# Optimization experiments

Hardware: AMD Instinct MI355X
Metric: run time of the kernel (lower is better)

The kernel has to match this reference:

```python
import jax, jax.numpy as jnp
import numpy as np
from jax import lax

DIM = 192; K = 3; SHARE_PLANES = 8
B = 2; D = 16; H = 32; W = 32
GROUPS_W = DIM * K * K // SHARE_PLANES // (K ** 3)   # 8 dynamic-weight groups
SHARE = DIM // GROUPS_W                              # 24 channels share each group
GN_GROUPS = DIM // SHARE_PLANES                      # 24 GroupNorm groups over 216 ch
ATTN = max(DIM * 2 // 4, 32)                         # 96 SE hidden channels
EPS = 1e-5


def setup_inputs() -> dict:
    key = jax.random.key(0)
    ks = jax.random.split(key, 24)
    rn = lambda k, sh, s=0.05: jax.random.normal(k, sh, jnp.float32) * s
    sc = lambda k, sh: 1.0 + jax.random.uniform(k, sh, jnp.float32) * 0.1
    return {
        'x':      jax.random.normal(ks[0], (B, DIM, D, H, W), jnp.float32),
        'w_key':  rn(ks[1], (DIM, DIM // 4, K, K, K)),
        'bn1_s':  sc(ks[2], (DIM,)),  'bn1_b': rn(ks[3], (DIM,)),
        'w_e1':   rn(ks[4], (DIM // 2, 2 * DIM)),
        'bn2_s':  sc(ks[5], (DIM // 2,)), 'bn2_b': rn(ks[6], (DIM // 2,)),
        'w_e2':   rn(ks[7], (K * K * DIM // SHARE_PLANES, DIM // 2)),
        'b_e2':   rn(ks[8], (K * K * DIM // SHARE_PLANES,)),
        'gn_s':   sc(ks[9], (K * K * DIM // SHARE_PLANES,)),
        'gn_b':   rn(ks[10], (K * K * DIM // SHARE_PLANES,)),
        'w_c1':   rn(ks[11], (DIM, DIM)),
        'bn3_s':  sc(ks[12], (DIM,)), 'bn3_b': rn(ks[13], (DIM,)),
        'bn4_s':  sc(ks[14], (DIM,)), 'bn4_b': rn(ks[15], (DIM,)),
        'w_se1':  rn(ks[16], (ATTN, DIM)), 'b_se1': rn(ks[17], (ATTN,)),
        'bnse_s': sc(ks[18], (ATTN,)), 'bnse_b': rn(ks[19], (ATTN,)),
        'w_se2':  rn(ks[20], (2 * DIM, ATTN)), 'b_se2': rn(ks[21], (2 * DIM,)),
    }


def _bn5(t, s, b):  # eval-mode BatchNorm3d folded to per-channel affine
    return t * s[None, :, None, None, None] + b[None, :, None, None, None]


def _conv1x1(w, t):  # pointwise Conv3d as contraction over channels
    return jnp.einsum('oi,bidhw->bodhw', w, t)


def reference(x, w_key, bn1_s, bn1_b, w_e1, bn2_s, bn2_b, w_e2, b_e2, gn_s, gn_b,
              w_c1, bn3_s, bn3_b, bn4_s, bn4_b, w_se1, b_se1, bnse_s, bnse_b,
              w_se2, b_se2):
    # key embedding: grouped 3x3x3 conv + BN + ReLU
    k = lax.conv_general_dilated(x, w_key, (1, 1, 1), 'SAME',
                                 dimension_numbers=('NCDHW', 'OIDHW', 'NCDHW'),
                                 feature_group_count=4)
    k = jax.nn.relu(_bn5(k, bn1_s, bn1_b))

    qk = jnp.concatenate([x, k], axis=1)                    # [B, 2C, D, H, W]
    e = jax.nn.relu(_bn5(_conv1x1(w_e1, qk), bn2_s, bn2_b)) # [B, C/2, D, H, W]
    w = _conv1x1(w_e2, e) + b_e2[None, :, None, None, None] # [B, 216, D, H, W]

    # GroupNorm over 24 groups of 9 channels
    b_, cw, d_, h_, w_ = w.shape
    wg = w.reshape(b_, GN_GROUPS, cw // GN_GROUPS, d_, h_, w_)
    mu = wg.mean(axis=(2, 3, 4, 5), keepdims=True)
    var = wg.var(axis=(2, 3, 4, 5), keepdims=True)
    w = ((wg - mu) * lax.rsqrt(var + EPS)).reshape(b_, cw, d_, h_, w_)
    w = w * gn_s[None, :, None, None, None] + gn_b[None, :, None, None, None]

    # dynamic per-pixel weights: [B, G=8, K^3=27, D, H, W]
    wdyn = w.reshape(b_, GROUPS_W, K ** 3, d_, h_, w_)

    v = _bn5(_conv1x1(w_c1, x), bn3_s, bn3_b)               # values [B, C, D, H, W]

    # LocalConvolution (involution): accumulate over 27 shifts, never
    # materializing the full [B, C, 27, D, H, W] unfold.
    pad = (K - 1) // 2
    vpad = jnp.pad(v, ((0, 0), (0, 0), (pad, pad), (pad, pad), (pad, pad)))
    out = jnp.zeros_like(v)
    idx = 0
    for dz in range(K):
        for dy in range(K):
            for dx in range(K):
                patch = vpad[:, :, dz:dz + d_, dy:dy + h_, dx:dx + w_]
                wk = jnp.repeat(wdyn[:, :, idx], SHARE, axis=1)  # [B, C, D, H, W]
                out = out + wk * patch
                idx += 1

    x2 = _bn5(out, bn4_s, bn4_b)
    x2 = x2 * jax.nn.sigmoid(x2)                             # swish

    stacked = jnp.stack([x2, k], axis=2)                     # [B, C, radix=2, D, H, W]
    gap = stacked.sum(axis=2).mean(axis=(2, 3, 4))           # [B, C]
    h1 = jax.nn.relu((jnp.einsum('oi,bi->bo', w_se1, gap) + b_se1) * bnse_s + bnse_b)
    attn = jnp.einsum('oi,bi->bo', w_se2, h1) + b_se2        # [B, 2C]
    attn = jax.nn.softmax(attn.reshape(b_, DIM, 2), axis=2)
    return (stacked * attn[:, :, :, None, None, None]).sum(axis=2)
```

## Files before the change

### kernel.cpp

```cpp
#include <hip/hip_runtime.h>
#include <hip/hip_bf16.h>
#include <cstdint>

#define SP 16384

typedef __attribute__((ext_vector_type(8))) short bf16x8;
typedef __attribute__((ext_vector_type(4))) short bf16x4;
typedef __attribute__((ext_vector_type(4))) float f32x4;

__device__ inline unsigned short f2bf(float f) {
  unsigned u = __float_as_uint(f);
  unsigned r = (u + 0x7FFFu + ((u >> 16) & 1u)) >> 16;
  return (unsigned short)r;
}
__device__ inline float bf2f(unsigned short h) {
  return __uint_as_float(((unsigned)h) << 16);
}

__global__ __launch_bounds__(256) void prep_w(const float* __restrict__ wkey,
                                              unsigned short* __restrict__ apk)
{
  int e = blockIdx.x * 256 + threadIdx.x;
  int ic8 = e & 7;
  int t4 = (e >> 3) & 3;
  int rest = e >> 5;
  int oc = rest % 48;  int rest2 = rest / 48;
  int tapch = rest2 % 7; int rest3 = rest2 / 7;
  int icch = rest3 % 6; int g = rest3 / 6;
  int tap = tapch * 4 + t4;
  float v = 0.f;
  if (tap < 27)
    v = wkey[((size_t)(g * 48 + oc) * 48 + icch * 8 + ic8) * 27 + tap];
  apk[e] = f2bf(v);
}

__global__ __launch_bounds__(256) void prep_x(const float* __restrict__ x,
                                              unsigned short* __restrict__ actbf)
{
  int t = blockIdx.x * 256 + threadIdx.x;
  int n = t & 16383;
  int v = t >> 14;
  int cc = v % 24, b = v / 24;
  bf16x8 pk;
  #pragma unroll
  for (int i = 0; i < 8; ++i)
    pk[i] = (short)f2bf(x[(((size_t)b * 192 + cc * 8 + i) << 14) + n]);
  *(bf16x8*)&actbf[((size_t)(b * 48 + cc) * 16384 + n) * 8] = pk;
}

__global__ __launch_bounds__(256) void pack_a(const float* __restrict__ src,
                                              unsigned short* __restrict__ dst,
                                              int M, int K)
{
  int e = blockIdx.x * 256 + threadIdx.x;
  int j = e & 7, lh = (e >> 3) & 3, r = (e >> 5) & 15;
  int rest = e >> 9;
  int KCH = K >> 5;
  int kc = rest % KCH, mf = rest / KCH;
  int m = mf * 16 + r, k = kc * 32 + lh * 8 + j;
  dst[e] = (m < M) ? f2bf(src[(size_t)m * K + k]) : (unsigned short)0;
}

__global__ __launch_bounds__(256) void k1_mfma(
    const unsigned short* __restrict__ actbf_in, const unsigned short* __restrict__ apk,
    const float* __restrict__ bn1s, const float* __restrict__ bn1b,
    float* __restrict__ kout, unsigned short* __restrict__ actbf_out)
{
  const int tile = blockIdx.x;
  const int g = blockIdx.y;
  const int b = blockIdx.z;
  const int z0 = (tile >> 3) * 2, y0 = (tile & 7) * 4;
  const int tid = threadIdx.x;
  const int lane = tid & 63, wid = tid >> 6;
  const int ln = lane & 15, lh = lane >> 4;

  __shared__ __align__(16) unsigned short xs[4 * 6 * 34 * 8];

  int offT[7];
  #pragma unroll
  for (int tc = 0; tc < 7; ++tc) {
    int tap = tc * 4 + lh; if (tap > 26) tap = 26;
    int dz = tap / 9, r = tap - dz * 9, dy = r / 3, dx = r - dy * 3;
    offT[tc] = dz * 1632 + dy * 272 + dx * 8;
  }
  const int zw = wid >> 1, yb = (wid & 1) * 2;
  int bbase[4];
  #pragma unroll
  for (int f = 0; f < 4; ++f)
    bbase[f] = zw * 1632 + (yb + (f >> 1)) * 272 + ((f & 1) * 16 + ln) * 8;

  f32x4 acc[3][4];
  #pragma unroll
  for (int m = 0; m < 3; ++m)
    #pragma unroll
    for (int f = 0; f < 4; ++f) { f32x4 z4 = {0.f, 0.f, 0.f, 0.f}; acc[m][f] = z4; }

  const unsigned short* ag = apk + (size_t)g * 6 * 7 * 1536;

  for (int icch = 0; icch < 6; ++icch) {
    __syncthreads();
    const unsigned short* xsrc = actbf_in + ((size_t)(b * 48 + g * 6 + icch) * 16384) * 8;
    for (int e = tid; e < 816; e += 256) {
      int row = e / 34, xr = e - row * 34;
      int zz = row / 6, yy = row - zz * 6;
      int gz = z0 - 1 + zz, gy = y0 - 1 + yy, gx = xr - 1;
      bf16x8 v = {0, 0, 0, 0, 0, 0, 0, 0};
      if ((unsigned)gz < 16u && (unsigned)gy < 32u && (unsigned)gx < 32u)
        v = *(const bf16x8*)&xsrc[((gz << 10) + (gy << 5) + gx) * 8];
      *(bf16x8*)&xs[row * 272 + xr * 8] = v;
    }
    __syncthreads();
    const unsigned short* ab = ag + (size_t)icch * 7 * 1536;
    #pragma unroll
    for (int tc = 0; tc < 7; ++tc) {
      bf16x8 a0 = *(const bf16x8*)&ab[tc * 1536 + (0 * 16 + ln) * 32 + lh * 8];
      bf16x8 a1 = *(const bf16x8*)&ab[tc * 1536 + (1 * 16 + ln) * 32 + lh * 8];
      bf16x8 a2 = *(const bf16x8*)&ab[tc * 1536 + (2 * 16 + ln) * 32 + lh * 8];
      bf16x8 bb[4];
      #pragma unroll
      for (int f = 0; f < 4; ++f) bb[f] = *(const bf16x8*)&xs[bbase[f] + offT[tc]];
      #pragma unroll
      for (int f = 0; f < 4; ++f) {
        acc[0][f] = __builtin_amdgcn_mfma_f32_16x16x32_bf16(a0, bb[f], acc[0][f], 0, 0, 0);
        acc[1][f] = __builtin_amdgcn_mfma_f32_16x16x32_bf16(a1, bb[f], acc[1][f], 0, 0, 0);
        acc[2][f] = __builtin_amdgcn_mfma_f32_16x16x32_bf16(a2, bb[f], acc[2][f], 0, 0, 0);
      }
    }
  }
  const int z = z0 + zw;
  #pragma unroll
  for (int mf = 0; mf < 3; ++mf) {
    #pragma unroll
    for (int f = 0; f < 4; ++f) {
      const int y = y0 + yb + (f >> 1);
      const int xq = (f & 1) * 16 + ln;
      const int n = (z << 10) + (y << 5) + xq;
      unsigned short h4[4];
      #pragma unroll
      for (int r = 0; r < 4; ++r) {
        int oc = g * 48 + mf * 16 + lh * 4 + r;
        float t = fmaxf(acc[mf][f][r] * bn1s[oc] + bn1b[oc], 0.f);
        kout[(((size_t)b * 192 + oc) << 14) + n] = t;
        h4[r] = f2bf(t);
      }
      int cc = 24 + g * 6 + mf * 2 + (lh >> 1);
      bf16x4 hv = {(short)h4[0], (short)h4[1], (short)h4[2], (short)h4[3]};
      *(bf16x4*)&actbf_out[((size_t)(b * 48 + cc) * 16384 + n) * 8 + (lh & 1) * 4] = hv;
    }
  }
}

template<int KCH, int MT, int EPI, int SPLITB, int BPL>
__global__ __launch_bounds__(256) void gemm_mfma(
    const unsigned short* __restrict__ apk,
    const unsigned short* __restrict__ bact,
    const float* __restrict__ sc, const float* __restrict__ bi,
    float* __restrict__ outf, unsigned short* __restrict__ outbf,
    int Mfull)
{
  const int b = blockIdx.z;
  const int tid = threadIdx.x;
  const int lane = tid & 63, wid = tid >> 6;
  const int ln = lane & 15, lh = lane >> 4;
  const int n = blockIdx.x * 64 + wid * 16 + ln;

  f32x4 acc[MT];
  #pragma unroll
  for (int m = 0; m < MT; ++m) { f32x4 z = {0.f, 0.f, 0.f, 0.f}; acc[m] = z; }

  const unsigned short* bb = bact + ((size_t)(b * BPL + lh) * 16384 + n) * 8;
  #pragma unroll
  for (int kc = 0; kc < KCH; ++kc) {
    bf16x8 bfr = *(const bf16x8*)(bb + (size_t)kc * 4 * 131072);
    bf16x8 bfr2;
    if (SPLITB) bfr2 = *(const bf16x8*)(bb + 3145728 + (size_t)kc * 4 * 131072);
    #pragma unroll
    for (int m = 0; m < MT; ++m) {
      bf16x8 afr = *(const bf16x8*)&apk[(((m * KCH + kc) * 16 + ln) * 4 + lh) * 8];
      acc[m] = __builtin_amdgcn_mfma_f32_16x16x32_bf16(afr, bfr, acc[m], 0, 0, 0);
      if (SPLITB)
        acc[m] = __builtin_amdgcn_mfma_f32_16x16x32_bf16(afr, bfr2, acc[m], 0, 0, 0);
    }
  }
  #pragma unroll
  for (int m = 0; m < MT; ++m) {
    int c0 = m * 16 + lh * 4;
    if (EPI == 0) {
      unsigned short h[4], l[4];
      #pragma unroll
      for (int r = 0; r < 4; ++r) {
        int c = c0 + r;
        float t = fmaxf(acc[m][r] * sc[c] + bi[c], 0.f);
        h[r] = f2bf(t);
        l[r] = f2bf(t - bf2f(h[r]));
      }
      int cc = m * 2 + (lh >> 1);
      size_t o = ((size_t)(b * 12 + cc) * 16384 + n) * 8 + (lh & 1) * 4;
      bf16x4 hv = {(short)h[0], (short)h[1], (short)h[2], (short)h[3]};
      bf16x4 lv = {(short)l[0], (short)l[1], (short)l[2], (short)l[3]};
      *(bf16x4*)&outbf[o] = hv;
      *(bf16x4*)&outbf[o + 3145728] = lv;
    } else {
      #pragma unroll
      for (int r = 0; r < 4; ++r) {
        int c = c0 + r;
        if (EPI == 2 && c >= Mfull) continue;
        float t = (EPI == 1) ? (acc[m][r] * sc[c] + bi[c]) : (acc[m][r] + bi[c]);
        outf[(((size_t)b * Mfull + c) << 14) + n] = t;
      }
    }
  }
}

__global__ __launch_bounds__(256) void k3b_gnstats(const float* __restrict__ wraw,
                                                   float* __restrict__ gsums)
{
  const int chunk = blockIdx.x, g = blockIdx.y, b = blockIdx.z;
  const float4* p = (const float4*)(wraw + (((size_t)b * 216 + g * 9) << 14));
  float s1 = 0.f, s2 = 0.f;
  const int base = chunk * 4608 + threadIdx.x;
  #pragma unroll 4
  for (int i = 0; i < 18; ++i) {
    float4 v = p[base + i * 256];
    s1 += v.x + v.y + v.z + v.w;
    s2 += v.x * v.x + v.y * v.y + v.z * v.z + v.w * v.w;
  }
  #pragma unroll
  for (int o = 32; o > 0; o >>= 1) { s1 += __shfl_down(s1, o); s2 += __shfl_down(s2, o); }
  __shared__ float ps[4][2];
  int lane = threadIdx.x & 63, w = threadIdx.x >> 6;
  if (lane == 0) { ps[w][0] = s1; ps[w][1] = s2; }
  __syncthreads();
  if (threadIdx.x == 0) {
    float t1 = ps[0][0] + ps[1][0] + ps[2][0] + ps[3][0];
    float t2 = ps[0][1] + ps[1][1] + ps[2][1] + ps[3][1];
    atomicAdd(&gsums[(b * 24 + g) * 2 + 0], t1);
    atomicAdd(&gsums[(b * 24 + g) * 2 + 1], t2);
  }
}

__global__ __launch_bounds__(256) void k4_dynconv(
    const float* __restrict__ wraw, const float* __restrict__ vbuf,
    const float* __restrict__ gsums,
    const float* __restrict__ gns, const float* __restrict__ gnb,
    const float* __restrict__ bn4s, const float* __restrict__ bn4b,
    float* __restrict__ x2)
{
  const int tile = blockIdx.x;
  const int z0 = (tile >> 2) * 4, y0 = (tile & 3) * 8;
  const int cs = blockIdx.y;
  const int b = blockIdx.z >> 3, gw = blockIdx.z & 7;
  const int tid = threadIdx.x;
  const int tx = (tid & 7) * 4, ty = (tid >> 3) & 7, tz = tid >> 6;

  __shared__ __align__(16) float vs[6][6][10][35];
  __shared__ __align__(16) float wls[3][1024];

  float mu[3], rs[3];
  #pragma unroll
  for (int j = 0; j < 3; ++j) {
    int gr = gw * 3 + j;
    float m1 = gsums[(b * 24 + gr) * 2 + 0] * (1.f / 147456.f);
    float m2 = gsums[(b * 24 + gr) * 2 + 1] * (1.f / 147456.f);
    mu[j] = m1;
    rs[j] = rsqrtf(m2 - m1 * m1 + 1e-5f);
  }
  const int c0 = gw * 24 + cs * 6;
  for (int e = tid; e < 6 * 2040; e += 256) {
    int cc = e / 2040; int r = e - cc * 2040;
    int zz = r / 340;  int r2 = r - zz * 340;
    int yy = r2 / 34;  int xx = r2 - yy * 34;
    int gz = z0 - 1 + zz, gy = y0 - 1 + yy, gx = xx - 1;
    float val = 0.f;
    if (gz >= 0 && gz < 16 && gy >= 0 && gy < 32 && gx >= 0 && gx < 32)
      val = vbuf[(((size_t)b * 192 + c0 + cc) << 14) + (gz << 10) + (gy << 5) + gx];
    vs[cc][zz][yy][xx] = val;
  }
  float acc[6][4] = {};
  for (int chnk = 0; chnk < 9; ++chnk) {
    const int dz = chnk / 3, dy = chnk - dz * 3;
    __syncthreads();
    #pragma unroll
    for (int i = 0; i < 3; ++i) {
      int e4 = tid + i * 256;
      int idxi = e4 >> 8, s4 = e4 & 255;
      int zz = s4 >> 6, rem = s4 & 63, yy = rem >> 3, x4 = rem & 7;
      int cw = gw * 27 + chnk * 3 + idxi;
      float scw = rs[dz] * gns[cw];
      float shw = gnb[cw] - mu[dz] * scw;
      float4 wv = *(const float4*)&wraw[(((size_t)b * 216 + cw) << 14) +
                                        ((z0 + zz) << 10) + ((y0 + yy) << 5) + (x4 << 2)];
      float4 o4;
      o4.x = wv.x * scw + shw; o4.y = wv.y * scw + shw;
      o4.z = wv.z * scw + shw; o4.w = wv.w * scw + shw;
      int row = zz * 8 + yy;
      ((float4*)&wls[idxi][0])[(row << 3) | (x4 ^ (row & 7))] = o4;
    }
    __syncthreads();
    float xv[6][6];
    #pragma unroll
    for (int cc = 0; cc < 6; ++cc)
      #pragma unroll
      for (int j = 0; j < 6; ++j) xv[cc][j] = vs[cc][tz + dz][ty + dy][tx + j];
    const int row = tz * 8 + ty;
    #pragma unroll
    for (int dxi = 0; dxi < 3; ++dxi) {
      float4 wv = ((const float4*)&wls[dxi][0])[(row << 3) | ((tx >> 2) ^ (row & 7))];
      float w4[4] = {wv.x, wv.y, wv.z, wv.w};
      #pragma unroll
      for (int cc = 0; cc < 6; ++cc)
        #pragma unroll
        for (int xi = 0; xi < 4; ++xi)
          acc[cc][xi] += w4[xi] * xv[cc][dxi + xi];
    }
  }
  #pragma unroll
  for (int cc = 0; cc < 6; ++cc) {
    int c = c0 + cc;
    float scv = bn4s[c], bb = bn4b[c];
    float4 r;
    float t;
    t = acc[cc][0] * scv + bb; r.x = t / (1.f + expf(-t));
    t = acc[cc][1] * scv + bb; r.y = t / (1.f + expf(-t));
    t = acc[cc][2] * scv + bb; r.z = t / (1.f + expf(-t));
    t = acc[cc][3] * scv + bb; r.w = t / (1.f + expf(-t));
    *(float4*)&x2[(((size_t)b * 192 + c) << 14) + ((z0 + tz) << 10) + ((y0 + ty) << 5) + tx] = r;
  }
}

__global__ __launch_bounds__(256) void k5a_gap(const float* __restrict__ x2,
                                               const float* __restrict__ k,
                                               float* __restrict__ gap)
{
  const int bc = blockIdx.x;
  const float4* p1 = (const float4*)(x2 + ((size_t)bc << 14));
  const float4* p2 = (const float4*)(k + ((size_t)bc << 14));
  float s = 0.f;
  for (int i = threadIdx.x; i < 4096; i += 256) {
    float4 a = p1[i], b2 = p2[i];
    s += (a.x + b2.x) + (a.y + b2.y) + (a.z + b2.z) + (a.w + b2.w);
  }
  #pragma unroll
  for (int o = 32; o > 0; o >>= 1) s += __shfl_down(s, o);
  __shared__ float ps[4];
  if ((threadIdx.x & 63) == 0) ps[threadIdx.x >> 6] = s;
  __syncthreads();
  if (threadIdx.x == 0) gap[bc] = (ps[0] + ps[1] + ps[2] + ps[3]) * (1.f / 16384.f);
}

__global__ __launch_bounds__(256) void k5b_se(
    const float* __restrict__ gap,
    const float* __restrict__ wse1, const float* __restrict__ bse1,
    const float* __restrict__ bnses, const float* __restrict__ bnseb,
    const float* __restrict__ wse2, const float* __restrict__ bse2,
    float* __restrict__ attnb)
{
  __shared__ float g[384];
  __shared__ float h[192];
  __shared__ float at[768];
  const int tid = threadIdx.x;
  for (int t = tid; t < 384; t += 256) g[t] = gap[t];
  __syncthreads();
  if (tid < 192) {
    int b = tid / 96, o = tid - b * 96;
    float s = 0.f;
    for (int i = 0; i < 192; ++i) s += wse1[o * 192 + i] * g[b * 192 + i];
    s = (s + bse1[o]) * bnses[o] + bnseb[o];
    h[tid] = fmaxf(s, 0.f);
  }
  __syncthreads();
  for (int t = tid; t < 768; t += 256) {
    int b = t / 384, o = t - b * 384;
    float s = 0.f;
    for (int i = 0; i < 96; ++i) s += wse2[o * 96 + i] * h[b * 96 + i];
    at[t] = s + bse2[o];
  }
  __syncthreads();
  for (int t = tid; t < 384; t += 256) {
    int b = t / 192, c = t - b * 192;
    float a0 = at[b * 384 + 2 * c], a1 = at[b * 384 + 2 * c + 1];
    float m = fmaxf(a0, a1);
    float e0 = expf(a0 - m), e1 = expf(a1 - m);
    float inv = 1.f / (e0 + e1);
    attnb[t * 2 + 0] = e0 * inv;
    attnb[t * 2 + 1] = e1 * inv;
  }
}

__global__ __launch_bounds__(256) void k6_combine(const float* __restrict__ k,
                                                  const float* __restrict__ attnb,
                                                  float* io)
{
  const int i4 = blockIdx.x * 256 + threadIdx.x;
  const int bc = i4 >> 12;
  float p0 = attnb[bc * 2 + 0], p1 = attnb[bc * 2 + 1];
  float4 a = ((const float4*)io)[i4];
  float4 kk = ((const float4*)k)[i4];
  float4 r;
  r.x = a.x * p0 + kk.x * p1;
  r.y = a.y * p0 + kk.y * p1;
  r.z = a.z * p0 + kk.z * p1;
  r.w = a.w * p0 + kk.w * p1;
  ((float4*)io)[i4] = r;
}

extern "C" void kernel_launch(void* const* d_in, const int* in_sizes, int n_in,
                              void* d_out, int out_size, void* d_ws, size_t ws_size,
                              hipStream_t stream) {
  const float* x     = (const float*)d_in[0];
  const float* wkey  = (const float*)d_in[1];
  const float* bn1s  = (const float*)d_in[2];
  const float* bn1b  = (const float*)d_in[3];
  const float* we1   = (const float*)d_in[4];
  const float* bn2s  = (const float*)d_in[5];
  const float* bn2b  = (const float*)d_in[6];
  const float* we2   = (const float*)d_in[7];
  const float* be2   = (const float*)d_in[8];
  const float* gns   = (const float*)d_in[9];
  const float* gnb   = (const float*)d_in[10];
  const float* wc1   = (const float*)d_in[11];
  const float* bn3s  = (const float*)d_in[12];
  const float* bn3b  = (const float*)d_in[13];
  const float* bn4s  = (const float*)d_in[14];
  const float* bn4b  = (const float*)d_in[15];
  const float* wse1  = (const float*)d_in[16];
  const float* bse1  = (const float*)d_in[17];
  const float* bnses = (const float*)d_in[18];
  const float* bnseb = (const float*)d_in[19];
  const float* wse2  = (const float*)d_in[20];
  const float* bse2  = (const float*)d_in[21];

  float* ws = (float*)d_ws;
  float* kbuf           = ws;
  float* vbuf           = ws + 6291456;
  unsigned short* ebf   = (unsigned short*)(ws + 12582912);
  unsigned short* actbf = (unsigned short*)(ws + 15728640);
  float* wrbuf          = ws + 15728640;
  unsigned short* apk1  = (unsigned short*)(ws + 22806528);
  unsigned short* apkV  = (unsigned short*)(ws + 22935552);
  unsigned short* apkE  = (unsigned short*)(ws + 22953984);
  unsigned short* apkW  = (unsigned short*)(ws + 22972416);
  float* gsums          = ws + 22983168;
  float* gap            = ws + 22983264;
  float* attnb          = ws + 22983648;
  float* x2             = (float*)d_out;

  hipMemsetAsync(gsums, 0, 96 * sizeof(float), stream);

  prep_w<<<dim3(1008), 256, 0, stream>>>(wkey, apk1);
  prep_x<<<dim3(3072), 256, 0, stream>>>(x, actbf);
  pack_a<<<dim3(144), 256, 0, stream>>>(wc1, apkV, 192, 192);
  pack_a<<<dim3(144), 256, 0, stream>>>(we1, apkE, 96, 384);
  pack_a<<<dim3(84), 256, 0, stream>>>(we2, apkW, 224, 96);

  k1_mfma<<<dim3(64, 4, 2), 256, 0, stream>>>(actbf, apk1, bn1s, bn1b, kbuf, actbf);
  gemm_mfma<6, 12, 1, 0, 48><<<dim3(256, 1, 2), 256, 0, stream>>>(
      apkV, actbf, bn3s, bn3b, vbuf, nullptr, 192);
  gemm_mfma<12, 6, 0, 0, 48><<<dim3(256, 1, 2), 256, 0, stream>>>(
      apkE, actbf, bn2s, bn2b, nullptr, ebf, 96);
  gemm_mfma<3, 14, 2, 1, 12><<<dim3(256, 1, 2), 256, 0, stream>>>(
      apkW, ebf, nullptr, be2, wrbuf, nullptr, 216);

  k3b_gnstats<<<dim3(8, 24, 2), 256, 0, stream>>>(wrbuf, gsums);
  k4_dynconv<<<dim3(16, 4, 16), 256, 0, stream>>>(wrbuf, vbuf, gsums, gns, gnb, bn4s, bn4b, x2);
  k5a_gap<<<dim3(384), 256, 0, stream>>>(x2, kbuf, gap);
  k5b_se<<<dim3(1), 256, 0, stream>>>(gap, wse1, bse1, bnses, bnseb, wse2, bse2, attnb);
  k6_combine<<<dim3(6144), 256, 0, stream>>>(kbuf, attnb, (float*)d_out);
}
```

Before: 314.8 us.

## Load dynamic weights directly into registers and drop per-chunk LDS staging

The dynamic-conv kernel no longer stages the normalized per-tap weights through shared memory for each of the 9 (dz,dy) chunks. Each thread now reads its own float4 of raw weights from global memory and applies the GroupNorm affine in registers. This removes 18 block barriers and the LDS round trip. The value tile row is padded to 36 floats so the x window can be read with aligned float4 LDS loads, and the chunk loop is fully unrolled. In exchange there are more registers per thread and global loads that no longer overlap behind a barrier.

```diff
diff --git a/kernel.cpp b/kernel.cpp
--- a/kernel.cpp
+++ b/kernel.cpp
@@ -253,8 +253,7 @@
   const int tid = threadIdx.x;
   const int tx = (tid & 7) * 4, ty = (tid >> 3) & 7, tz = tid >> 6;
 
-  __shared__ __align__(16) float vs[6][6][10][35];
-  __shared__ __align__(16) float wls[3][1024];
+  __shared__ __align__(16) float vs[6][6][10][36];
 
   float mu[3], rs[3];
   #pragma unroll
@@ -276,37 +275,35 @@
       val = vbuf[(((size_t)b * 192 + c0 + cc) << 14) + (gz << 10) + (gy << 5) + gx];
     vs[cc][zz][yy][xx] = val;
   }
+  __syncthreads();
+
+  const float* wp = wraw + (((size_t)b * 216 + gw * 27) << 14) +
+                    ((z0 + tz) << 10) + ((y0 + ty) << 5) + tx;
+
   float acc[6][4] = {};
+  #pragma unroll
   for (int chnk = 0; chnk < 9; ++chnk) {
     const int dz = chnk / 3, dy = chnk - dz * 3;
-    __syncthreads();
-    #pragma unroll
-    for (int i = 0; i < 3; ++i) {
-      int e4 = tid + i * 256;
-      int idxi = e4 >> 8, s4 = e4 & 255;
-      int zz = s4 >> 6, rem = s4 & 63, yy = rem >> 3, x4 = rem & 7;
-      int cw = gw * 27 + chnk * 3 + idxi;
-      float scw = rs[dz] * gns[cw];
-      float shw = gnb[cw] - mu[dz] * scw;
-      float4 wv = *(const float4*)&wraw[(((size_t)b * 216 + cw) << 14) +
-                                        ((z0 + zz) << 10) + ((y0 + yy) << 5) + (x4 << 2)];
-      float4 o4;
-      o4.x = wv.x * scw + shw; o4.y = wv.y * scw + shw;
-      o4.z = wv.z * scw + shw; o4.w = wv.w * scw + shw;
-      int row = zz * 8 + yy;
-      ((float4*)&wls[idxi][0])[(row << 3) | (x4 ^ (row & 7))] = o4;
-    }
-    __syncthreads();
-    float xv[6][6];
-    #pragma unroll
-    for (int cc = 0; cc < 6; ++cc)
-      #pragma unroll
-      for (int j = 0; j < 6; ++j) xv[cc][j] = vs[cc][tz + dz][ty + dy][tx + j];
-    const int row = tz * 8 + ty;
+    float4 wv0 = *(const float4*)(wp + ((size_t)(chnk * 3 + 0) << 14));
+    float4 wv1 = *(const float4*)(wp + ((size_t)(chnk * 3 + 1) << 14));
+    float4 wv2 = *(const float4*)(wp + ((size_t)(chnk * 3 + 2) << 14));
+    float xv[6][8];
+    #pragma unroll
+    for (int cc = 0; cc < 6; ++cc) {
+      float4 xa = *(const float4*)&vs[cc][tz + dz][ty + dy][tx];
+      float4 xb = *(const float4*)&vs[cc][tz + dz][ty + dy][tx + 4];
+      xv[cc][0] = xa.x; xv[cc][1] = xa.y; xv[cc][2] = xa.z; xv[cc][3] = xa.w;
+      xv[cc][4] = xb.x; xv[cc][5] = xb.y; xv[cc][6] = xb.z; xv[cc][7] = xb.w;
+    }
     #pragma unroll
     for (int dxi = 0; dxi < 3; ++dxi) {
-      float4 wv = ((const float4*)&wls[dxi][0])[(row << 3) | ((tx >> 2) ^ (row & 7))];
-      float w4[4] = {wv.x, wv.y, wv.z, wv.w};
+      const int cw = gw * 27 + chnk * 3 + dxi;
+      const float scw = rs[dz] * gns[cw];
+      const float shw = gnb[cw] - mu[dz] * scw;
+      float4 wv = (dxi == 0) ? wv0 : (dxi == 1) ? wv1 : wv2;
+      float w4[4];
+      w4[0] = wv.x * scw + shw; w4[1] = wv.y * scw + shw;
+      w4[2] = wv.z * scw + shw; w4[3] = wv.w * scw + shw;
       #pragma unroll
       for (int cc = 0; cc < 6; ++cc)
         #pragma unroll
```

Measured after the change: 308.1 us. -2.1%, faster.
